# Kernel optimization log

Hardware: AMD Instinct MI355X
Metric: run time of the kernel (lower is better)

## Reference

```python
import jax, jax.numpy as jnp
import numpy as np

B, N, DIM = 4, 2048, 768
H, C = 12, 64            # num_heads, head_dim
M = 384                  # num random features = dim * kernel_ratio
SCALE = C ** (-0.25)
EPS = 1e-8
INV_SQRT_M = 1.0 / np.sqrt(M).astype(np.float32)


def _make_orf(key):
    # per-head orthogonal random features: rows of each (C, M) block are
    # orthonormal (C <= M), scaled by sqrt(M), matching sample_orf's intent.
    g = jax.random.normal(key, (H, M, C), jnp.float32)
    q = jnp.linalg.qr(g)[0]                 # (H, M, C), orthonormal columns
    return jnp.transpose(q, (0, 2, 1)) * np.float32(np.sqrt(M))  # (H, C, M)


def setup_inputs() -> dict:
    key = jax.random.key(0)
    k0, k1, k2, k3 = jax.random.split(key, 4)
    x = jax.random.normal(k0, (B, N, DIM), jnp.float32)
    w = _make_orf(k1)                                       # (H, C, M), frozen
    Wqkv = jax.random.normal(k2, (DIM, 3 * DIM), jnp.float32) * 0.02
    Wproj = jax.random.normal(k3, (DIM, DIM), jnp.float32) * 0.02
    bproj = jnp.zeros((DIM,), jnp.float32)
    return {"x": x, "w": w, "Wqkv": Wqkv, "Wproj": Wproj, "bproj": bproj}


def _kernel(x, w):
    # x: (B, H, N, C) -> phi(x): (B, H, N, M)
    xs = x * SCALE
    proj = jnp.einsum('bhnc,hcm->bhnm', xs, w)
    sq_half = 0.5 * jnp.sum(xs * xs, axis=-1, keepdims=True)  # (B,H,N,1)
    return jnp.exp(proj - sq_half) * INV_SQRT_M


def reference(x, w, Wqkv, Wproj, bproj):
    qkv = (x @ Wqkv).reshape(B, N, 3, H, C).transpose(2, 0, 3, 1, 4)
    q, k, v = qkv[0], qkv[1], qkv[2]
    qf = _kernel(q, w)                       # (B, H, N, M)
    kf = _kernel(k, w)                       # (B, H, N, M)
    # normalizer D_n = q'_n . sum_j k'_j
    D = jnp.einsum('bhnm,bhm->bhn', qf, jnp.sum(kf, axis=2)) + EPS
    # linear attention: (k'^T v) then q' @ (k'^T v)
    ktv = jnp.einsum('bhnm,bhnc->bhmc', kf, v)      # (B, H, M, C)
    out = jnp.einsum('bhnm,bhmc->bhnc', qf, ktv) / D[..., None]
    out = out.transpose(0, 2, 1, 3).reshape(B, N, DIM)
    return out @ Wproj + bproj
```

## Files before the change

### kernel.cpp

```cpp
#include <hip/hip_runtime.h>

typedef __attribute__((ext_vector_type(8))) short s16x8;
typedef __attribute__((ext_vector_type(4))) float f32x4;

#define MFMA(a, b, c) __builtin_amdgcn_mfma_f32_16x16x32_bf16(a, b, c, 0, 0, 0)

namespace {

constexpr int Bn = 4, Nn = 2048, Hn = 12, Mn = 384;
constexpr float SCALE = 0.35355339059327379f;
constexpr float EPS = 1e-8f;
constexpr float SC2 = 0.51012051755958393f;
constexpr float SQC2 = 0.090169742829486635f;

__device__ inline unsigned short f2b(float f) {
  unsigned u = __builtin_bit_cast(unsigned, f);
  return (unsigned short)((u + 0x7fffu + ((u >> 16) & 1u)) >> 16);
}
__device__ inline float b2f(unsigned short h) {
  unsigned u = ((unsigned)h) << 16;
  return __builtin_bit_cast(float, u);
}

__device__ inline void gl_lds16(const unsigned short* g, unsigned short* l) {
  __builtin_amdgcn_global_load_lds(
      (const __attribute__((address_space(1))) unsigned int*)g,
      (__attribute__((address_space(3))) unsigned int*)l, 16, 0, 0);
}

__device__ inline void tr_cvt_64(const float* __restrict__ src, int sld,
                                 unsigned short* __restrict__ dst, int dld,
                                 float* lds ) {
  const int t = threadIdx.x;
  const int r = t >> 4, cq = (t & 15) * 4;
#pragma unroll
  for (int p = 0; p < 4; ++p) {
    const int k = p * 16 + r;
    const float4 v = *(const float4*)(src + (size_t)k * sld + cq);
    lds[k * 65 + cq + 0] = v.x;
    lds[k * 65 + cq + 1] = v.y;
    lds[k * 65 + cq + 2] = v.z;
    lds[k * 65 + cq + 3] = v.w;
  }
  __syncthreads();
  const int n = t >> 2, kq = (t & 3) * 16;
  s16x8 o0, o1;
#pragma unroll
  for (int j = 0; j < 8; ++j) {
    o0[j] = (short)f2b(lds[(kq + j) * 65 + n]);
    o1[j] = (short)f2b(lds[(kq + 8 + j) * 65 + n]);
  }
  *(s16x8*)(dst + (size_t)n * dld + kq) = o0;
  *(s16x8*)(dst + (size_t)n * dld + kq + 8) = o1;
}

__global__ __launch_bounds__(256) void cvt_all_k(const float* __restrict__ x,
                                                 const float* __restrict__ Wqkv,
                                                 const float* __restrict__ Wproj,
                                                 const float* __restrict__ w,
                                                 unsigned short* __restrict__ xb,
                                                 unsigned short* __restrict__ wqT,
                                                 unsigned short* __restrict__ wpT,
                                                 unsigned short* __restrict__ wt) {
  __shared__ float lds[64 * 65];
  const int bid = blockIdx.x;
  if (bid < 3072) {
    const int id = bid * 256 + threadIdx.x;
    const float* src = x + (size_t)id * 8;
    s16x8 o;
#pragma unroll
    for (int j = 0; j < 8; ++j) o[j] = (short)f2b(src[j]);
    *(s16x8*)(xb + (size_t)id * 8) = o;
  } else if (bid < 3504) {
    const int tid = bid - 3072;
    const int k0 = (tid % 12) * 64, n0 = (tid / 12) * 64;
    tr_cvt_64(Wqkv + (size_t)k0 * 2304 + n0, 2304, wqT + (size_t)n0 * 768 + k0, 768, lds);
  } else if (bid < 3648) {
    const int tid = bid - 3504;
    const int k0 = (tid % 12) * 64, n0 = (tid / 12) * 64;
    tr_cvt_64(Wproj + (size_t)k0 * 768 + n0, 768, wpT + (size_t)n0 * 768 + k0, 768, lds);
  } else {
    const int tid = bid - 3648;
    const int h = tid / 6, m0 = (tid % 6) * 64;
    tr_cvt_64(w + (size_t)h * 64 * 384 + m0, 384, wt + ((size_t)h * 384 + m0) * 64, 64, lds);
  }
}

__global__ __launch_bounds__(256) void gemm_qkv_k(const unsigned short* __restrict__ A,
                                                  const unsigned short* __restrict__ Bt,
                                                  unsigned short* __restrict__ obf) {
  __shared__ unsigned short ldsA[128 * 64];
  __shared__ unsigned short ldsB[128 * 64];
  char* lA = (char*)ldsA;
  char* lB = (char*)ldsB;
  const int t = threadIdx.x, lane = t & 63, w = t >> 6;
  const int ln = lane & 15, kg = lane >> 4;
  const int flat = blockIdx.y * 18 + blockIdx.x;
  const int swz = (flat & 7) * 144 + (flat >> 3);
  const size_t bm = (size_t)(swz / 18) * 128, bn = (size_t)(swz % 18) * 128;
  const int wr = w >> 1, wc = w & 1;
  const int sr = lane >> 3, s = lane & 7;
  f32x4 acc[4][4];
#pragma unroll
  for (int i = 0; i < 4; ++i)
#pragma unroll
    for (int j = 0; j < 4; ++j) acc[i][j] = (f32x4){0.f, 0.f, 0.f, 0.f};

  for (int kb = 0; kb < 768; kb += 64) {
    __syncthreads();
#pragma unroll
    for (int c = 0; c < 4; ++c) {
      const int row = c * 32 + w * 8 + sr;
      const int ss = (s ^ (row & 7)) * 8;
      gl_lds16(A + (bm + row) * 768 + kb + ss, ldsA + (c * 4 + w) * 512);
      gl_lds16(Bt + (bn + row) * 768 + kb + ss, ldsB + (c * 4 + w) * 512);
    }
    __syncthreads();
#pragma unroll
    for (int ks = 0; ks < 2; ++ks) {
      s16x8 af[4], bfr[4];
#pragma unroll
      for (int mi = 0; mi < 4; ++mi) {
        const int row = wr * 64 + mi * 16 + ln;
        af[mi] = *(const s16x8*)(lA + row * 128 + (((ks * 4 + kg) ^ (row & 7)) << 4));
      }
#pragma unroll
      for (int ni = 0; ni < 4; ++ni) {
        const int row = wc * 64 + ni * 16 + ln;
        bfr[ni] = *(const s16x8*)(lB + row * 128 + (((ks * 4 + kg) ^ (row & 7)) << 4));
      }
#pragma unroll
      for (int mi = 0; mi < 4; ++mi)
#pragma unroll
        for (int ni = 0; ni < 4; ++ni) acc[mi][ni] = MFMA(af[mi], bfr[ni], acc[mi][ni]);
    }
  }
#pragma unroll
  for (int mi = 0; mi < 4; ++mi)
#pragma unroll
    for (int ni = 0; ni < 4; ++ni) {
      const size_t orow0 = bm + wr * 64 + mi * 16 + kg * 4;
      const size_t ocol = bn + wc * 64 + ni * 16 + ln;
#pragma unroll
      for (int r = 0; r < 4; ++r) obf[(orow0 + r) * 2304 + ocol] = f2b(acc[mi][ni][r]);
    }
}

__global__ __launch_bounds__(256) void gemm_proj_k(const unsigned short* __restrict__ A,
                                                   const unsigned short* __restrict__ Bt,
                                                   float* __restrict__ out,
                                                   const float* __restrict__ bias) {
  __shared__ unsigned short ldsA[128 * 64];
  __shared__ unsigned short ldsB[64 * 64];
  char* lA = (char*)ldsA;
  char* lB = (char*)ldsB;
  const int t = threadIdx.x, lane = t & 63, w = t >> 6;
  const int ln = lane & 15, kg = lane >> 4;
  const int flat = blockIdx.y * 12 + blockIdx.x;
  const int swz = (flat & 7) * 96 + (flat >> 3);
  const size_t bm = (size_t)(swz / 12) * 128, bn = (size_t)(swz % 12) * 64;
  const int wr = w >> 1, wc = w & 1;
  const int sr = lane >> 3, s = lane & 7;
  f32x4 acc[4][2];
#pragma unroll
  for (int i = 0; i < 4; ++i)
#pragma unroll
    for (int j = 0; j < 2; ++j) acc[i][j] = (f32x4){0.f, 0.f, 0.f, 0.f};

  for (int kb = 0; kb < 768; kb += 64) {
    __syncthreads();
#pragma unroll
    for (int c = 0; c < 4; ++c) {
      const int row = c * 32 + w * 8 + sr;
      const int ss = (s ^ (row & 7)) * 8;
      gl_lds16(A + (bm + row) * 768 + kb + ss, ldsA + (c * 4 + w) * 512);
    }
#pragma unroll
    for (int c = 0; c < 2; ++c) {
      const int row = c * 32 + w * 8 + sr;
      const int ss = (s ^ (row & 7)) * 8;
      gl_lds16(Bt + (bn + row) * 768 + kb + ss, ldsB + (c * 4 + w) * 512);
    }
    __syncthreads();
#pragma unroll
    for (int ks = 0; ks < 2; ++ks) {
      s16x8 af[4], bfr[2];
#pragma unroll
      for (int mi = 0; mi < 4; ++mi) {
        const int row = wr * 64 + mi * 16 + ln;
        af[mi] = *(const s16x8*)(lA + row * 128 + (((ks * 4 + kg) ^ (row & 7)) << 4));
      }
#pragma unroll
      for (int ni = 0; ni < 2; ++ni) {
        const int row = wc * 32 + ni * 16 + ln;
        bfr[ni] = *(const s16x8*)(lB + row * 128 + (((ks * 4 + kg) ^ (row & 7)) << 4));
      }
#pragma unroll
      for (int mi = 0; mi < 4; ++mi)
#pragma unroll
        for (int ni = 0; ni < 2; ++ni) acc[mi][ni] = MFMA(af[mi], bfr[ni], acc[mi][ni]);
    }
  }
#pragma unroll
  for (int mi = 0; mi < 4; ++mi)
#pragma unroll
    for (int ni = 0; ni < 2; ++ni) {
      const size_t orow0 = bm + wr * 64 + mi * 16 + kg * 4;
      const size_t ocol = bn + wc * 32 + ni * 16 + ln;
      const float bv = bias[ocol];
#pragma unroll
      for (int r = 0; r < 4; ++r) out[(orow0 + r) * 768 + ocol] = acc[mi][ni][r] + bv;
    }
}

template <int NCT, int CT0>
__device__ inline void s2_gemm2(const char* kfT_b, const char* vt_b, int mts, int ln, int kg,
                                f32x4 (*acc)[3]) {
#pragma unroll
  for (int half = 0; half < 2; ++half) {
    s16x8 a[3], bb[NCT];
#pragma unroll
    for (int j = 0; j < 3; ++j) {
      const int m = (mts + j) * 16 + ln;
      a[j] = *(const s16x8*)(kfT_b + m * 128 + ((half * 64 + kg * 16) ^ ((m & 7) << 4)));
    }
#pragma unroll
    for (int i = 0; i < NCT; ++i) {
      const int c = (CT0 + i) * 16 + ln;
      bb[i] = *(const s16x8*)(vt_b + c * 128 + ((half * 64 + kg * 16) ^ ((c & 7) << 4)));
    }
#pragma unroll
    for (int j = 0; j < 3; ++j)
#pragma unroll
      for (int i = 0; i < NCT; ++i) acc[j][i] = MFMA(a[j], bb[i], acc[j][i]);
  }
}

__global__ __launch_bounds__(512, 4) void stage2_k(const unsigned short* __restrict__ qkv,
                                                   const unsigned short* __restrict__ wt,
                                                   float* __restrict__ ktv_part,
                                                   float* __restrict__ ksum_part) {
  __shared__ unsigned short kfT[192 * 64];
  __shared__ unsigned short vt[2][80 * 64];
  __shared__ unsigned short wt_s[192 * 64];
  __shared__ unsigned short k_s[64 * 64];
  char* kfT_b = (char*)kfT;
  char* wt_b = (char*)wt_s;
  char* k_b = (char*)k_s;
  const int t = threadIdx.x, lane = t & 63, w = t >> 6;
  const int ln = lane & 15, kg = lane >> 4;
  const int gx = blockIdx.x, h = blockIdx.y, b = blockIdx.z;
  const int ng = gx >> 1, mh = gx & 1, m0 = mh * 192;
  const int bh = b * Hn + h;
  const int ntile = w & 3, mgrp = w >> 2;
  const int mts = (w & 3) * 3;
  const int cg = w >> 2;
  const int lr = lane >> 3, sl = lane & 7;

  auto stage_k = [&](int ch) {
    const int row = w * 8 + lr;
    gl_lds16(qkv + ((size_t)b * Nn + ng * 512 + ch * 64 + row) * 2304 + 768 + h * 64 +
                 ((sl ^ (row & 7)) * 8),
             k_s + w * 512);
  };
  const int vn = t >> 3, vc0 = (t & 7) * 8;
  auto load_v = [&](int ch) {
    return *(const s16x8*)(qkv + ((size_t)b * Nn + ng * 512 + ch * 64 + vn) * 2304 + 1536 +
                           h * 64 + vc0);
  };
  auto scat_v = [&](s16x8 vv, int buf) {
    char* vb = (char*)vt[buf];
#pragma unroll
    for (int j = 0; j < 8; ++j) {
      const int c = vc0 + j;
      *(unsigned short*)(vb + c * 128 + ((2 * vn) ^ ((c & 7) << 4))) = (unsigned short)vv[j];
    }
  };

#pragma unroll
  for (int rr = 0; rr < 3; ++rr) {
    const int j = w * 3 + rr;
    const int row = j * 8 + lr;
    gl_lds16(wt + ((size_t)h * 384 + m0 + row) * 64 + ((sl ^ (row & 7)) * 8), wt_s + j * 512);
  }
  for (int i = t; i < 2048; i += 512) {
    const int buf = i >> 10, r = i & 1023;
    const int c = 64 + (r >> 6), nn = r & 63;
    *(unsigned short*)((char*)vt[buf] + c * 128 + ((2 * nn) ^ ((c & 7) << 4))) =
        (c == 64) ? (unsigned short)0x3F80 : (unsigned short)0;
  }
  stage_k(0);
  s16x8 vreg = load_v(0);
  __syncthreads();
  scat_v(vreg, 0);
  __syncthreads();

  f32x4 acc[3][3];
#pragma unroll
  for (int j = 0; j < 3; ++j)
#pragma unroll
    for (int i = 0; i < 3; ++i) acc[j][i] = (f32x4){0.f, 0.f, 0.f, 0.f};

  for (int ch = 0; ch < 8; ++ch) {
    {
      const int arow = ntile * 16 + ln;
      const s16x8 a0 = *(const s16x8*)(k_b + arow * 128 + ((kg ^ (arow & 7)) << 4));
      const s16x8 a1 = *(const s16x8*)(k_b + arow * 128 + (((kg + 4) ^ (arow & 7)) << 4));
      float sq = 0.f;
#pragma unroll
      for (int j = 0; j < 8; ++j) {
        const float f0 = b2f((unsigned short)a0[j]);
        const float f1 = b2f((unsigned short)a1[j]);
        sq = fmaf(f0, f0, sq);
        sq = fmaf(f1, f1, sq);
      }
      sq += __shfl_xor(sq, 16);
      sq += __shfl_xor(sq, 32);
      const int kg4 = (lane >> 4) << 2;
      float sqv[4];
#pragma unroll
      for (int r = 0; r < 4; ++r) sqv[r] = SQC2 * __shfl(sq, kg4 + r);
#pragma unroll
      for (int i = 0; i < 6; ++i) {
        const int mloc = (mgrp * 6 + i) * 16 + ln;
        const s16x8 b0 = *(const s16x8*)(wt_b + mloc * 128 + ((kg ^ (mloc & 7)) << 4));
        const s16x8 b1 = *(const s16x8*)(wt_b + mloc * 128 + (((kg + 4) ^ (mloc & 7)) << 4));
        f32x4 p = (f32x4){0.f, 0.f, 0.f, 0.f};
        p = MFMA(a0, b0, p);
        p = MFMA(a1, b1, p);
        const float e0 = exp2f(fmaf(SC2, p[0], -sqv[0]));
        const float e1 = exp2f(fmaf(SC2, p[1], -sqv[1]));
        const float e2 = exp2f(fmaf(SC2, p[2], -sqv[2]));
        const float e3 = exp2f(fmaf(SC2, p[3], -sqv[3]));
        uint2 pk;
        pk.x = (unsigned)f2b(e0) | ((unsigned)f2b(e1) << 16);
        pk.y = (unsigned)f2b(e2) | ((unsigned)f2b(e3) << 16);
        const int bytn = 32 * ntile + 8 * kg;
        *(uint2*)(kfT_b + mloc * 128 + (bytn ^ ((mloc & 7) << 4))) = pk;
      }
    }
    __syncthreads();
    if (ch < 7) {
      stage_k(ch + 1);
      vreg = load_v(ch + 1);
    }
    const char* vt_cur = (const char*)vt[ch & 1];
    if (cg == 0)
      s2_gemm2<3, 0>(kfT_b, vt_cur, mts, ln, kg, acc);
    else
      s2_gemm2<2, 3>(kfT_b, vt_cur, mts, ln, kg, acc);
    if (ch < 7) scat_v(vreg, (ch + 1) & 1);
    __syncthreads();
  }
  float* base = ktv_part + ((size_t)ng * 48 + bh) * (384 * 64);
  const int nct2 = cg ? 2 : 3, ct0c = cg ? 3 : 0;
#pragma unroll
  for (int j = 0; j < 3; ++j)
#pragma unroll
    for (int i = 0; i < 3; ++i) {
      if (i >= nct2) continue;
      const int ct = ct0c + i;
      const int mrow0 = m0 + (mts + j) * 16 + kg * 4;
      if (ct < 4) {
        const int c = ct * 16 + ln;
#pragma unroll
        for (int r = 0; r < 4; ++r) base[(size_t)(mrow0 + r) * 64 + c] = acc[j][i][r];
      } else if (ln == 0) {
#pragma unroll
        for (int r = 0; r < 4; ++r)
          ksum_part[((size_t)ng * 48 + bh) * 384 + mrow0 + r] = acc[j][i][r];
      }
    }
}

__global__ __launch_bounds__(256) void reduce_all_k(const float* __restrict__ part,
                                                    const float* __restrict__ partk,
                                                    unsigned short* __restrict__ ktve) {
  const int bid = blockIdx.x;
  if (bid < 4608) {
    const int bh = bid / 96, chunk = bid % 96;
    const int idx = chunk * 256 + threadIdx.x;
    const int m = idx >> 6, c = idx & 63;
    const size_t o = (size_t)bh * 24576 + idx;
    const size_t gs = (size_t)48 * 24576;
    const float s = part[o] + part[o + gs] + part[o + 2 * gs] + part[o + 3 * gs];
    ktve[((size_t)bh * 80 + c) * 384 + m] = f2b(s);
  } else {
    const int idx = (bid - 4608) * 256 + threadIdx.x;
    const int bh = idx / 384, m = idx % 384;
    const int gk = 48 * 384;
    const float s = partk[idx] + partk[idx + gk] + partk[idx + 2 * gk] + partk[idx + 3 * gk];
    const unsigned short hi = f2b(s);
    const unsigned short lo = f2b(s - b2f(hi));
    const size_t base = ((size_t)bh * 80 + 64) * 384 + m;
    ktve[base] = hi;
    ktve[base + 384] = lo;
  }
}

__global__ __launch_bounds__(512, 4) void stage3_k(const unsigned short* __restrict__ qkv,
                                                   const unsigned short* __restrict__ wt,
                                                   const unsigned short* __restrict__ ktve,
                                                   unsigned short* __restrict__ attn) {
  __shared__ unsigned short q_s[128 * 64];
  __shared__ unsigned short qf_s[128 * 64];
  __shared__ unsigned short wt_s[2][64 * 64];
  __shared__ unsigned short kt_s[2][80 * 64];
  char* q_b = (char*)q_s;
  char* qf_b = (char*)qf_s;
  const int t = threadIdx.x, lane = t & 63, w = t >> 6;
  const int ln = lane & 15, kg = lane >> 4;
  const int nb = blockIdx.x, h = blockIdx.y, b = blockIdx.z, bh = b * Hn + h;
  const size_t tok0 = (size_t)b * Nn + nb * 128;
  const int lr = lane >> 3, sl = lane & 7;

#pragma unroll
  for (int rr = 0; rr < 2; ++rr) {
    const int row = w * 16 + rr * 8 + lr;
    gl_lds16(qkv + (tok0 + row) * 2304 + h * 64 + ((sl ^ (row & 7)) * 8),
             q_s + (w * 16 + rr * 8) * 64 + lane * 8);
  }
  auto stage_wt = [&](int mc, int pb) {
    const int row = w * 8 + lr;
    gl_lds16(wt + ((size_t)h * 384 + mc * 64 + row) * 64 + ((sl ^ (row & 7)) * 8),
             wt_s[pb] + w * 512 + lane * 8);
  };
  auto stage_kt = [&](int mc, int pb) {
    const int row = w * 8 + lr;
    gl_lds16(ktve + ((size_t)bh * 80 + row) * 384 + mc * 64 + ((sl ^ (row & 7)) * 8),
             kt_s[pb] + w * 512 + lane * 8);
    if (w < 2) {
      const int row2 = 64 + w * 8 + lr;
      gl_lds16(ktve + ((size_t)bh * 80 + row2) * 384 + mc * 64 + ((sl ^ (row2 & 7)) * 8),
               kt_s[pb] + (64 + w * 8) * 64 + lane * 8);
    }
  };
  stage_wt(0, 0);
  stage_kt(0, 0);
  __syncthreads();

  f32x4 acc2[5];
#pragma unroll
  for (int i = 0; i < 5; ++i) acc2[i] = (f32x4){0.f, 0.f, 0.f, 0.f};

  const int arow = w * 16 + ln;
  const char* qrow = q_b + arow * 128;
  const int asw = (arow & 7) << 4;

  for (int mc = 0; mc < 6; ++mc) {
    const int pb = mc & 1;
    if (mc < 5) {
      stage_wt(mc + 1, pb ^ 1);
      stage_kt(mc + 1, pb ^ 1);
    }
    const s16x8 af0 = *(const s16x8*)(qrow + ((kg << 4) ^ asw));
    const s16x8 af1 = *(const s16x8*)(qrow + (((kg + 4) << 4) ^ asw));
    const char* wb = (const char*)wt_s[pb];
    f32x4 p[4];
#pragma unroll
    for (int mt = 0; mt < 4; ++mt) {
      const int mrow = mt * 16 + ln;
      const s16x8 b0 = *(const s16x8*)(wb + mrow * 128 + ((kg ^ (mrow & 7)) << 4));
      const s16x8 b1 = *(const s16x8*)(wb + mrow * 128 + (((kg + 4) ^ (mrow & 7)) << 4));
      f32x4 pp = (f32x4){0.f, 0.f, 0.f, 0.f};
      pp = MFMA(af0, b0, pp);
      p[mt] = MFMA(af1, b1, pp);
    }
#pragma unroll
    for (int mt = 0; mt < 4; ++mt) {
#pragma unroll
      for (int r = 0; r < 4; ++r) {
        const int trow = w * 16 + kg * 4 + r;
        const int m = mt * 16 + ln;
        *(unsigned short*)(qf_b + trow * 128 + ((2 * m) ^ ((trow & 7) << 4))) =
            f2b(exp2f(SC2 * p[mt][r]));
      }
    }
    const char* qfr = qf_b + arow * 128;
    const s16x8 a0 = *(const s16x8*)(qfr + ((kg << 4) ^ asw));
    const s16x8 a1 = *(const s16x8*)(qfr + (((kg + 4) << 4) ^ asw));
    const char* kb = (const char*)kt_s[pb];
#pragma unroll
    for (int ct = 0; ct < 5; ++ct) {
      const int crow = ct * 16 + ln;
      const s16x8 b0 = *(const s16x8*)(kb + crow * 128 + ((kg ^ (crow & 7)) << 4));
      const s16x8 b1 = *(const s16x8*)(kb + crow * 128 + (((kg + 4) ^ (crow & 7)) << 4));
      acc2[ct] = MFMA(a0, b0, acc2[ct]);
      acc2[ct] = MFMA(a1, b1, acc2[ct]);
    }
    __syncthreads();
  }
  float dv[4];
#pragma unroll
  for (int r = 0; r < 4; ++r) {
    const float hi = __shfl(acc2[4][r], (lane & 48));
    const float lo = __shfl(acc2[4][r], (lane & 48) | 1);
    dv[r] = 1.0f / (hi + lo + EPS);
  }
#pragma unroll
  for (int ct = 0; ct < 4; ++ct) {
#pragma unroll
    for (int r = 0; r < 4; ++r) {
      const int trow = w * 16 + kg * 4 + r;
      const int c = ct * 16 + ln;
      attn[(tok0 + trow) * 768 + h * 64 + c] = f2b(acc2[ct][r] * dv[r]);
    }
  }
}

}

extern "C" void kernel_launch(void* const* d_in, const int* in_sizes, int n_in,
                              void* d_out, int out_size, void* d_ws, size_t ws_size,
                              hipStream_t stream) {
  const float* x = (const float*)d_in[0];
  const float* w = (const float*)d_in[1];
  const float* Wqkv = (const float*)d_in[2];
  const float* Wproj = (const float*)d_in[3];
  const float* bproj = (const float*)d_in[4];

  char* ws = (char*)d_ws;
  unsigned short* xb = (unsigned short*)(ws);
  unsigned short* wqT = (unsigned short*)(ws + 12582912);
  float* ktv_part = (float*)(ws);
  float* ksum_part = (float*)(ws + 18874368);
  char* p = ws + 19169280;
  unsigned short* qkvb = (unsigned short*)p;  p += 37748736;
  unsigned short* wt = (unsigned short*)p;    p += 589824;
  unsigned short* ktve = (unsigned short*)p;  p += 2949120;
  unsigned short* attn = (unsigned short*)p;  p += 12582912;
  unsigned short* wpT = (unsigned short*)p;

  cvt_all_k<<<3720, 256, 0, stream>>>(x, Wqkv, Wproj, w, xb, wqT, wpT, wt);
  gemm_qkv_k<<<dim3(18, 64), 256, 0, stream>>>(xb, wqT, qkvb);
  stage2_k<<<dim3(8, 12, 4), 512, 0, stream>>>(qkvb, wt, ktv_part, ksum_part);
  reduce_all_k<<<4680, 256, 0, stream>>>(ktv_part, ksum_part, ktve);
  stage3_k<<<dim3(16, 12, 4), 512, 0, stream>>>(qkvb, wt, ktve, attn);
  gemm_proj_k<<<dim3(12, 64), 256, 0, stream>>>(attn, wpT, (float*)d_out, bproj);
}
```

Before: 137.0 us.

## Triple-buffer QKV GEMM with 256x128 tiles and async vmcnt pipelining

The QKV projection GEMM moves from 128x128 tiles with 256 threads to 256x128 tiles with 512 threads. Global-to-LDS loads are triple-buffered: each step issues loads two tiles ahead and uses explicit s_waitcnt vmcnt counts plus raw barriers, so memory latency overlaps with MFMA work instead of synchronising twice per k-step. This uses about 147KB of LDS, which allows only one block per CU. Separately, stage3 now stages only 8 of the 16 extra ktve rows, presumably the ones that hold real data.

```diff
diff --git a/kernel.cpp b/kernel.cpp
--- a/kernel.cpp
+++ b/kernel.cpp
@@ -86,36 +86,56 @@
   }
 }
 
-__global__ __launch_bounds__(256) void gemm_qkv_k(const unsigned short* __restrict__ A,
+__global__ __launch_bounds__(512) void gemm_qkv_k(const unsigned short* __restrict__ A,
                                                   const unsigned short* __restrict__ Bt,
                                                   unsigned short* __restrict__ obf) {
-  __shared__ unsigned short ldsA[128 * 64];
-  __shared__ unsigned short ldsB[128 * 64];
-  char* lA = (char*)ldsA;
-  char* lB = (char*)ldsB;
+  __shared__ unsigned short ldsA[3][256 * 64];
+  __shared__ unsigned short ldsB[3][128 * 64];
   const int t = threadIdx.x, lane = t & 63, w = t >> 6;
   const int ln = lane & 15, kg = lane >> 4;
   const int flat = blockIdx.y * 18 + blockIdx.x;
-  const int swz = (flat & 7) * 144 + (flat >> 3);
-  const size_t bm = (size_t)(swz / 18) * 128, bn = (size_t)(swz % 18) * 128;
+  const int swz = (flat & 7) * 72 + (flat >> 3);
+  const size_t bm = (size_t)(swz / 18) * 256, bn = (size_t)(swz % 18) * 128;
   const int wr = w >> 1, wc = w & 1;
-  const int sr = lane >> 3, s = lane & 7;
+  const int srow = t >> 3, sslot = t & 7;
   f32x4 acc[4][4];
 #pragma unroll
   for (int i = 0; i < 4; ++i)
 #pragma unroll
     for (int j = 0; j < 4; ++j) acc[i][j] = (f32x4){0.f, 0.f, 0.f, 0.f};
 
-  for (int kb = 0; kb < 768; kb += 64) {
-    __syncthreads();
-#pragma unroll
-    for (int c = 0; c < 4; ++c) {
-      const int row = c * 32 + w * 8 + sr;
-      const int ss = (s ^ (row & 7)) * 8;
-      gl_lds16(A + (bm + row) * 768 + kb + ss, ldsA + (c * 4 + w) * 512);
-      gl_lds16(Bt + (bn + row) * 768 + kb + ss, ldsB + (c * 4 + w) * 512);
-    }
-    __syncthreads();
+  auto stage = [&](int ti, int d) {
+    const int kb = ti * 64;
+#pragma unroll
+    for (int i = 0; i < 4; ++i) {
+      const int row = i * 64 + srow;
+      gl_lds16(A + (bm + row) * 768 + kb + ((sslot ^ (row & 7)) * 8),
+               &ldsA[d][i * 4096 + t * 8]);
+    }
+#pragma unroll
+    for (int i = 0; i < 2; ++i) {
+      const int row = i * 64 + srow;
+      gl_lds16(Bt + (bn + row) * 768 + kb + ((sslot ^ (row & 7)) * 8),
+               &ldsB[d][i * 4096 + t * 8]);
+    }
+  };
+
+  stage(0, 0);
+  stage(1, 1);
+  for (int ti = 0; ti < 12; ++ti) {
+    const int cur = ti % 3;
+    if (ti + 2 < 12) {
+      stage(ti + 2, (ti + 2) % 3);
+      asm volatile("s_waitcnt vmcnt(12)" ::: "memory");
+    } else if (ti == 10) {
+      asm volatile("s_waitcnt vmcnt(6)" ::: "memory");
+    } else {
+      asm volatile("s_waitcnt vmcnt(0)" ::: "memory");
+    }
+    __builtin_amdgcn_s_barrier();
+    asm volatile("" ::: "memory");
+    const char* lA = (const char*)ldsA[cur];
+    const char* lB = (const char*)ldsB[cur];
 #pragma unroll
     for (int ks = 0; ks < 2; ++ks) {
       s16x8 af[4], bfr[4];
@@ -134,6 +154,9 @@
 #pragma unroll
         for (int ni = 0; ni < 4; ++ni) acc[mi][ni] = MFMA(af[mi], bfr[ni], acc[mi][ni]);
     }
+    asm volatile("" ::: "memory");
+    __builtin_amdgcn_s_barrier();
+    asm volatile("" ::: "memory");
   }
 #pragma unroll
   for (int mi = 0; mi < 4; ++mi)
@@ -429,10 +452,10 @@
     const int row = w * 8 + lr;
     gl_lds16(ktve + ((size_t)bh * 80 + row) * 384 + mc * 64 + ((sl ^ (row & 7)) * 8),
              kt_s[pb] + w * 512 + lane * 8);
-    if (w < 2) {
-      const int row2 = 64 + w * 8 + lr;
+    if (w == 0) {
+      const int row2 = 64 + lr;
       gl_lds16(ktve + ((size_t)bh * 80 + row2) * 384 + mc * 64 + ((sl ^ (row2 & 7)) * 8),
-               kt_s[pb] + (64 + w * 8) * 64 + lane * 8);
+               kt_s[pb] + 64 * 64 + lane * 8);
     }
   };
   stage_wt(0, 0);
@@ -532,7 +555,7 @@
   unsigned short* wpT = (unsigned short*)p;
 
   cvt_all_k<<<3720, 256, 0, stream>>>(x, Wqkv, Wproj, w, xb, wqT, wpT, wt);
-  gemm_qkv_k<<<dim3(18, 64), 256, 0, stream>>>(xb, wqT, qkvb);
+  gemm_qkv_k<<<dim3(18, 32), 512, 0, stream>>>(xb, wqT, qkvb);
   stage2_k<<<dim3(8, 12, 4), 512, 0, stream>>>(qkvb, wt, ktv_part, ksum_part);
   reduce_all_k<<<4680, 256, 0, stream>>>(ktv_part, ksum_part, ktve);
   stage3_k<<<dim3(16, 12, 4), 512, 0, stream>>>(qkvb, wt, ktve, attn);
```

Measured after the change: 150.7 us. 10.0% more time.
